# Performance work log

Hardware: AMD Instinct MI355X
Metric: run time of the kernel (lower is better)

Reference implementation:

```python
import math
import jax, jax.numpy as jnp
import numpy as np

B, H, W, CP = 64, 512, 512, 400
HALF_X = W // 2          # int, matches width//2 in the original
HALF_Y = H / 2.0         # float, matches height/2 in the original
NPTS = CP // 2
PI = math.pi


def fix_radians(tt):
    # Faithful translation of: -relu(-(2pi - relu(-tt)), threshold=-2pi) + relu(tt)
    inner = -(2.0 * PI - jnp.maximum(-tt, 0.0))
    thr = jnp.where(inner > -2.0 * PI, inner, 0.0)  # keras relu with threshold=-2pi
    return -thr + jnp.maximum(tt, 0.0)


def half_contour(pred_norm):
    # pred_norm: [B, H, W] in [0, 1]
    pred1st = jnp.round(pred_norm[:, :, :HALF_X])          # [B, H, W/2]
    x1st = jnp.sum(pred1st, axis=2)                        # [B, H] column count per row
    xaux = jnp.clip(x1st, 0.0, 1.0)                        # relu(.., threshold=0, max_value=1)
    ythtop = HALF_Y - jnp.sum(xaux[:, :HALF_X], axis=1)    # [B]
    ythbottom = HALF_Y + jnp.sum(xaux[:, HALF_X:], axis=1) # [B]
    rows = jnp.arange(W, dtype=pred_norm.dtype)[None, :]   # [1, W] (H == W assumed by original)
    # relu(rows - top) + top == max(rows, top); then min with bottom
    y1st = jnp.minimum(jnp.maximum(rows, ythtop[:, None]), ythbottom[:, None])  # [B, W]
    # Original: x1st <- half_x - x1st, then cart2pol(x1st - half_x, y1st - half_y)
    xc = -x1st                                             # [B, H]
    yc = y1st - HALF_Y                                     # [B, W]
    r1st = jnp.sqrt(xc ** 2 + yc ** 2)                     # [B, H]
    tt1st = fix_radians(jnp.arctan2(yc, xc))               # [B, H]

    tt_new = (PI / 2.0) + jnp.arange(NPTS, dtype=pred_norm.dtype) * (PI / NPTS)  # [NPTS]

    # RBF angular smoothing (get_rbf_points), with periodic wraparound copies
    tt_1 = jnp.concatenate([tt1st - 2.0 * PI, tt1st, tt1st + 2.0 * PI], axis=1)  # [B, 3H]
    r_cat = jnp.concatenate([r1st, r1st, r1st], axis=1)                          # [B, 3H]
    d2 = (tt_1[:, :, None] - tt_new[None, None, :]) ** 2                         # [B, 3H, NPTS]
    d2 = jnp.minimum(d2, 1.0)
    wgt = jnp.exp(-100.0 * d2)                                                   # [B, 3H, NPTS]
    wgt = wgt / jnp.sum(wgt, axis=1, keepdims=True)
    r_new = jnp.einsum('bkn,bk->bn', wgt, r_cat)                                 # [B, NPTS]

    x_new = r_new * jnp.cos(tt_new)[None, :] + HALF_X
    y_new = r_new * jnp.sin(tt_new)[None, :] + HALF_Y
    return jnp.stack([x_new, y_new], axis=-1)              # [B, NPTS, 2]


def setup_inputs() -> dict:
    key = jax.random.key(0)
    inputs = jax.random.uniform(key, (B, H, W, 2), dtype=jnp.float32)
    return {"inputs": inputs}


def reference(inputs) -> jnp.ndarray:
    lvc = inputs[:, :, :, -1]                              # [B, H, W]
    mn = jnp.min(lvc, axis=(1, 2), keepdims=True)
    mx = jnp.max(lvc, axis=(1, 2), keepdims=True)
    lvc_norm = (lvc - mn) / (mx - mn)
    c1 = half_contour(lvc_norm)                            # [B, NPTS, 2]
    c2 = half_contour(lvc_norm[:, :, ::-1])                # mirrored half
    c2 = jnp.concatenate([float(H) - c2[:, :, :1], c2[:, :, 1:]], axis=-1)[:, ::-1, :]
    return jnp.concatenate([c1, c2], axis=1)               # [B, CP, 2]
```

## Files before the change

kernel.cpp:

```cpp
#include <hip/hip_runtime.h>
#include <math.h>
#include <float.h>

#define BB 64
#define HH 512
#define WW 512
#define NPTS 200

#define PMIN_OFF 0
#define PMAX_OFF 2048
#define CNT_OFF  4224

__global__ __launch_bounds__(256) void kminmax(const float* __restrict__ in,
                                               float* __restrict__ ws) {
    int bid = blockIdx.x;
    int b   = bid >> 5;
    int c   = bid & 31;
    int t   = threadIdx.x;
    const float4* base = (const float4*)in + (size_t)b * 131072 + (size_t)c * 4096;
    float vmin = FLT_MAX, vmax = -FLT_MAX;
#pragma unroll
    for (int i = 0; i < 16; ++i) {
        float4 v = base[i * 256 + t];
        vmin = fminf(vmin, fminf(v.y, v.w));
        vmax = fmaxf(vmax, fmaxf(v.y, v.w));
    }
    for (int m = 32; m >= 1; m >>= 1) {
        vmin = fminf(vmin, __shfl_xor(vmin, m, 64));
        vmax = fmaxf(vmax, __shfl_xor(vmax, m, 64));
    }
    __shared__ float smin[4], smax[4];
    int wv = t >> 6;
    if ((t & 63) == 0) { smin[wv] = vmin; smax[wv] = vmax; }
    __syncthreads();
    if (t == 0) {
        float a = fminf(fminf(smin[0], smin[1]), fminf(smin[2], smin[3]));
        float z = fmaxf(fmaxf(smax[0], smax[1]), fmaxf(smax[2], smax[3]));
        ws[PMIN_OFF + bid] = a;
        ws[PMAX_OFF + bid] = z;
    }
}

__global__ __launch_bounds__(256) void kcount(const float* __restrict__ in,
                                              float* __restrict__ ws) {
    int gwave = (blockIdx.x * 256 + threadIdx.x) >> 6;
    int lane  = threadIdx.x & 63;
    int b     = gwave >> 9;
    int row   = gwave & 511;

    float mn = ws[PMIN_OFF + b * 32 + (lane & 31)];
    float mx = ws[PMAX_OFF + b * 32 + (lane & 31)];
    for (int m = 16; m >= 1; m >>= 1) {
        mn = fminf(mn, __shfl_xor(mn, m, 64));
        mx = fmaxf(mx, __shfl_xor(mx, m, 64));
    }
    float den = mx - mn;

    const float4* base = (const float4*)in + ((size_t)(b * HH + row)) * 256;
    int cl = 0, cr = 0;
#pragma unroll
    for (int i = 0; i < 4; ++i) {
        float4 v = base[i * 64 + lane];
        float t0 = (v.y - mn) / den;
        float t1 = (v.w - mn) / den;
        int c = (int)rintf(t0) + (int)rintf(t1);
        if (i < 2) cl += c; else cr += c;
    }
    for (int m = 32; m >= 1; m >>= 1) {
        cl += __shfl_xor(cl, m, 64);
        cr += __shfl_xor(cr, m, 64);
    }
    if (lane == 0) {
        ws[CNT_OFF + (b * 2 + 0) * 512 + row] = (float)cl;
        ws[CNT_OFF + (b * 2 + 1) * 512 + row] = (float)cr;
    }
}

__global__ __launch_bounds__(512) void kcontour(const float* __restrict__ ws,
                                                float* __restrict__ out) {
    const float TWO_PI_F = 6.28318530717958647692f;
    const float PI_F     = 3.14159265358979323846f;
    int b2    = blockIdx.x >> 1;
    int phase = blockIdx.x & 1;
    int b     = b2 >> 1;
    int half  = b2 & 1;
    int tid   = threadIdx.x;
    int wv    = tid >> 6;
    int lane  = tid & 63;

    const float* cnt = ws + CNT_OFF + b2 * 512;

    __shared__ __align__(16) float s_tt[512];
    __shared__ __align__(16) float s_r[512];
    __shared__ float s_red[8];
    __shared__ float s_bc[3];

    float c0 = cnt[tid];
    int flag = (c0 >= 1.0f) ? 1 : 0;
    int fs = flag;
    for (int m = 32; m >= 1; m >>= 1) fs += __shfl_xor(fs, m, 64);
    if (lane == 0) s_red[wv] = (float)fs;
    __syncthreads();
    if (tid == 0) {
        s_bc[0] = 256.0f - (s_red[0] + s_red[1] + s_red[2] + s_red[3]);
        s_bc[1] = 256.0f + (s_red[4] + s_red[5] + s_red[6] + s_red[7]);
    }
    __syncthreads();
    float ythtop = s_bc[0], ythbottom = s_bc[1];

    {
        float y1 = fminf(fmaxf((float)tid, ythtop), ythbottom);
        float xc = -c0;
        float yc = y1 - 256.0f;
        float rr = sqrtf(xc * xc + yc * yc);
        float tt;
        if (c0 == 0.0f && yc == 0.0f) {
            tt = PI_F;
        } else {
            tt = atan2f(yc, xc);
            if (tt < 0.0f) tt += TWO_PI_F;
        }
        s_tt[tid] = tt;
        s_r[tid]  = rr;
        float sr = rr;
        for (int m = 32; m >= 1; m >>= 1) sr += __shfl_xor(sr, m, 64);
        if (lane == 0) s_red[wv] = sr;
    }
    __syncthreads();
    if (tid == 0)
        s_bc[2] = s_red[0] + s_red[1] + s_red[2] + s_red[3] +
                  s_red[4] + s_red[5] + s_red[6] + s_red[7];
    __syncthreads();
    float sumr = s_bc[2];

    const float4* ttv = (const float4*)s_tt;
    const float4* rrv = (const float4*)s_r;
    float4 ta = ttv[lane], tb = ttv[lane + 64];
    float4 ra = rrv[lane], rb = rrv[lane + 64];
    float tts[8] = {ta.x, ta.y, ta.z, ta.w, tb.x, tb.y, tb.z, tb.w};
    float rs[8]  = {ra.x, ra.y, ra.z, ra.w, rb.x, rb.y, rb.z, rb.w};

    int pbase = phase * 100;
    for (int p = pbase + wv; p < pbase + 100; p += 8) {
        float ttn = 1.5707963267948966f + (float)p * 0.015707963267948966f;

        float d2[8];
        float dmin = 1.0f;
#pragma unroll
        for (int i = 0; i < 8; ++i) {
            float d = tts[i] - ttn;
            d2[i] = fminf(d * d, 1.0f);
            dmin = fminf(dmin, d2[i]);
        }
        for (int m = 32; m >= 1; m >>= 1)
            dmin = fminf(dmin, __shfl_xor(dmin, m, 64));

        float num = 0.0f, den = 0.0f;
#pragma unroll
        for (int i = 0; i < 8; ++i) {
            float wg = __expf(-100.0f * (d2[i] - dmin));
            den += wg;
            num += wg * rs[i];
        }
        for (int m = 32; m >= 1; m >>= 1) {
            den += __shfl_xor(den, m, 64);
            num += __shfl_xor(num, m, 64);
        }

        float w1 = __expf(-100.0f * (1.0f - dmin));
        den += 1024.0f * w1;
        num += 2.0f * w1 * sumr;

        float rn   = num / den;
        float xnew = rn * cosf(ttn) + 256.0f;
        float ynew = rn * sinf(ttn) + 256.0f;

        if (lane == 0) {
            if (half == 0) {
                out[((size_t)b * 400 + p) * 2 + 0] = xnew;
                out[((size_t)b * 400 + p) * 2 + 1] = ynew;
            } else {
                int q = 399 - p;
                out[((size_t)b * 400 + q) * 2 + 0] = 512.0f - xnew;
                out[((size_t)b * 400 + q) * 2 + 1] = ynew;
            }
        }
    }
}

extern "C" void kernel_launch(void* const* d_in, const int* in_sizes, int n_in,
                              void* d_out, int out_size, void* d_ws, size_t ws_size,
                              hipStream_t stream) {
    const float* in  = (const float*)d_in[0];
    float*       out = (float*)d_out;
    float*       ws  = (float*)d_ws;

    kminmax <<<dim3(2048), dim3(256), 0, stream>>>(in, ws);
    kcount  <<<dim3(8192), dim3(256), 0, stream>>>(in, ws);
    kcontour<<<dim3(256),  dim3(512), 0, stream>>>(ws, out);
}
```

Measured before the change: 221.0 us.

## Stage bf16 copy of channel in minmax pass to shrink count-pass reads

```diff
diff --git a/kernel.cpp b/kernel.cpp
--- a/kernel.cpp
+++ b/kernel.cpp
@@ -10,6 +10,13 @@
 #define PMIN_OFF 0
 #define PMAX_OFF 2048
 #define CNT_OFF  4224
+#define CMP_OFF  69760
+
+__device__ __forceinline__ unsigned short f2bf(float f) {
+    unsigned u = __float_as_uint(f);
+    u += 0x7FFFu + ((u >> 16) & 1u);
+    return (unsigned short)(u >> 16);
+}
 
 __global__ __launch_bounds__(256) void kminmax(const float* __restrict__ in,
                                                float* __restrict__ ws) {
@@ -18,12 +25,17 @@
     int c   = bid & 31;
     int t   = threadIdx.x;
     const float4* base = (const float4*)in + (size_t)b * 131072 + (size_t)c * 4096;
+    ushort2* cbase = (ushort2*)(ws + CMP_OFF) + (size_t)b * 131072 + (size_t)c * 4096;
     float vmin = FLT_MAX, vmax = -FLT_MAX;
 #pragma unroll
     for (int i = 0; i < 16; ++i) {
         float4 v = base[i * 256 + t];
         vmin = fminf(vmin, fminf(v.y, v.w));
         vmax = fmaxf(vmax, fmaxf(v.y, v.w));
+        ushort2 u;
+        u.x = f2bf(v.y);
+        u.y = f2bf(v.w);
+        cbase[i * 256 + t] = u;
     }
     for (int m = 32; m >= 1; m >>= 1) {
         vmin = fminf(vmin, __shfl_xor(vmin, m, 64));
@@ -41,8 +53,7 @@
     }
 }
 
-__global__ __launch_bounds__(256) void kcount(const float* __restrict__ in,
-                                              float* __restrict__ ws) {
+__global__ __launch_bounds__(256) void kcount(float* __restrict__ ws) {
     int gwave = (blockIdx.x * 256 + threadIdx.x) >> 6;
     int lane  = threadIdx.x & 63;
     int b     = gwave >> 9;
@@ -56,23 +67,21 @@
     }
     float den = mx - mn;
 
-    const float4* base = (const float4*)in + ((size_t)(b * HH + row)) * 256;
-    int cl = 0, cr = 0;
-#pragma unroll
-    for (int i = 0; i < 4; ++i) {
-        float4 v = base[i * 64 + lane];
-        float t0 = (v.y - mn) / den;
-        float t1 = (v.w - mn) / den;
-        int c = (int)rintf(t0) + (int)rintf(t1);
-        if (i < 2) cl += c; else cr += c;
-    }
-    for (int m = 32; m >= 1; m >>= 1) {
-        cl += __shfl_xor(cl, m, 64);
-        cr += __shfl_xor(cr, m, 64);
-    }
+    const uint4* cmp = (const uint4*)(ws + CMP_OFF);
+    uint4 q = cmp[(size_t)b * 32768 + (size_t)row * 64 + lane];
+    unsigned wbits[4] = {q.x, q.y, q.z, q.w};
+    int c = 0;
+#pragma unroll
+    for (int k = 0; k < 4; ++k) {
+        float v0 = __uint_as_float(wbits[k] << 16);
+        float v1 = __uint_as_float(wbits[k] & 0xFFFF0000u);
+        c += (int)rintf((v0 - mn) / den) + (int)rintf((v1 - mn) / den);
+    }
+    int pk = (lane < 32) ? c : (c << 16);
+    for (int m = 32; m >= 1; m >>= 1) pk += __shfl_xor(pk, m, 64);
     if (lane == 0) {
-        ws[CNT_OFF + (b * 2 + 0) * 512 + row] = (float)cl;
-        ws[CNT_OFF + (b * 2 + 1) * 512 + row] = (float)cr;
+        ws[CNT_OFF + (b * 2 + 0) * 512 + row] = (float)(pk & 0xFFFF);
+        ws[CNT_OFF + (b * 2 + 1) * 512 + row] = (float)(pk >> 16);
     }
 }
 
@@ -96,8 +105,7 @@
     __shared__ float s_bc[3];
 
     float c0 = cnt[tid];
-    int flag = (c0 >= 1.0f) ? 1 : 0;
-    int fs = flag;
+    int fs = (c0 >= 1.0f) ? 1 : 0;
     for (int m = 32; m >= 1; m >>= 1) fs += __shfl_xor(fs, m, 64);
     if (lane == 0) s_red[wv] = (float)fs;
     __syncthreads();
@@ -155,23 +163,23 @@
         for (int m = 32; m >= 1; m >>= 1)
             dmin = fminf(dmin, __shfl_xor(dmin, m, 64));
 
-        float num = 0.0f, den = 0.0f;
+        float num = 0.0f, dsum = 0.0f;
 #pragma unroll
         for (int i = 0; i < 8; ++i) {
             float wg = __expf(-100.0f * (d2[i] - dmin));
-            den += wg;
-            num += wg * rs[i];
+            dsum += wg;
+            num  += wg * rs[i];
         }
         for (int m = 32; m >= 1; m >>= 1) {
-            den += __shfl_xor(den, m, 64);
-            num += __shfl_xor(num, m, 64);
+            dsum += __shfl_xor(dsum, m, 64);
+            num  += __shfl_xor(num,  m, 64);
         }
 
         float w1 = __expf(-100.0f * (1.0f - dmin));
-        den += 1024.0f * w1;
-        num += 2.0f * w1 * sumr;
-
-        float rn   = num / den;
+        dsum += 1024.0f * w1;
+        num  += 2.0f * w1 * sumr;
+
+        float rn   = num / dsum;
         float xnew = rn * cosf(ttn) + 256.0f;
         float ynew = rn * sinf(ttn) + 256.0f;
 
@@ -196,6 +204,6 @@
     float*       ws  = (float*)d_ws;
 
     kminmax <<<dim3(2048), dim3(256), 0, stream>>>(in, ws);
-    kcount  <<<dim3(8192), dim3(256), 0, stream>>>(in, ws);
+    kcount  <<<dim3(8192), dim3(256), 0, stream>>>(ws);
     kcontour<<<dim3(256),  dim3(512), 0, stream>>>(ws, out);
 }
```

After: 214.7 us. 2.8% less time.
